# Optimization experiments

Measured on AMD Instinct MI355X. Metric: run time of the kernel, lower is better.

Reference implementation:

```python
import jax, jax.numpy as jnp
import numpy as np


def setup_inputs() -> dict:
    key = jax.random.key(0)
    kq, kk, kv, kb = jax.random.split(key, 4)
    B, H, S, D = 2, 12, 2048, 64
    q = jax.random.normal(kq, (B, H, S, D), dtype=jnp.float32)
    k = jax.random.normal(kk, (B, H, S, D), dtype=jnp.float32)
    v = jax.random.normal(kv, (B, H, S, D), dtype=jnp.float32)
    # sorted block ids -> contiguous blocks along the sequence
    block_ids = jnp.sort(jax.random.randint(kb, (B, S), 0, 4), axis=-1)
    return {"q": q, "k": k, "v": v, "block_ids": block_ids}


def _ghostmax(scores):
    # softmax over [scores, 0]: an extra ghost logit of value 0
    m = jnp.maximum(jnp.max(scores, axis=-1, keepdims=True), 0.0)
    e = jnp.exp(scores - m)
    denom = jnp.sum(e, axis=-1, keepdims=True) + jnp.exp(-m)
    return e / denom


def reference(q, k, v, block_ids):
    B, H, S, D = q.shape
    scaling = 1.0 / jnp.sqrt(jnp.asarray(D, dtype=q.dtype))
    # [B,H,S,S] scores
    scores = jnp.einsum('bhqd,bhkd->bhqk', q, k) * scaling
    # block-causal mask: attend only within same block AND to past positions
    same_block = block_ids[:, :, None] == block_ids[:, None, :]          # [B,S,S]
    causal = jnp.arange(S)[:, None] >= jnp.arange(S)[None, :]            # [S,S]
    mask = (same_block & causal)[:, None, :, :]                          # [B,1,S,S]
    scores = scores + (1.0 - mask.astype(scores.dtype)) * (-1e9)
    weights = _ghostmax(scores)
    # dropout p=0.0 (eval) -> identity
    return jnp.einsum('bhqk,bhkd->bhqd', weights, v)
```

## Files before the change

### kernel.cpp

```cpp
#include <hip/hip_runtime.h>


constexpr int Bc = 2, Hc = 12, Sc = 2048, Dc = 64;
constexpr int QT    = 16;
constexpr int LPR   = 4;
constexpr int DSUB  = 16;
constexpr int KTILE = 16;

__device__ __forceinline__ float bf_lo(unsigned u) {
    union { unsigned i; float f; } c; c.i = u << 16; return c.f;
}
__device__ __forceinline__ float bf_hi(unsigned u) {
    union { unsigned i; float f; } c; c.i = u & 0xffff0000u; return c.f;
}
__device__ __forceinline__ void expand_store(float* dst, float4 raw) {
    const unsigned* u = (const unsigned*)&raw;
    float4 a, b;
    a.x = bf_lo(u[0]); a.y = bf_hi(u[0]); a.z = bf_lo(u[1]); a.w = bf_hi(u[1]);
    b.x = bf_lo(u[2]); b.y = bf_hi(u[2]); b.z = bf_lo(u[3]); b.w = bf_hi(u[3]);
    ((float4*)dst)[0] = a;
    ((float4*)dst)[1] = b;
}

__global__ void sniff_dtype(const unsigned* __restrict__ q, int* __restrict__ flag) {
    __shared__ int acc;
    const int tid = threadIdx.x;
    if (tid == 0) acc = 0;
    __syncthreads();
    const unsigned word = q[tid];
    const int e = (word >> 7) & 0xff;
    const bool plausible = (e >= 0x70) && (e <= 0x90);
    const unsigned long long mask = __ballot(plausible);
    if ((tid & 63) == 0) atomicAdd(&acc, __popcll(mask));
    __syncthreads();
    if (tid == 0) *flag = (acc >= 128) ? 1 : 0;
}

template <bool BF16_IN>
__device__ __forceinline__ void attn_body(
    const void* __restrict__ qv, const void* __restrict__ kv_,
    const void* __restrict__ vv, const int* __restrict__ bidg,
    float* __restrict__ outg)
{
    __shared__ __align__(16) float ks[KTILE][Dc];
    __shared__ __align__(16) float vs[KTILE][Dc];
    __shared__ int kb[KTILE];

    const int bh    = blockIdx.x;
    const int qt    = blockIdx.y;
    const int b     = bh / Hc;
    const int tid   = threadIdx.x;
    const int q0    = qt * QT;
    const int r     = q0 + (tid >> 2);
    const int dbase = (tid & 3) * DSUB;

    const int* brow   = bidg + b * Sc;
    const int  my_bid = brow[r];
    const int  bid0   = brow[q0];

    int lo = 0, hi = q0;
    while (lo < hi) {
        int mid = (lo + hi) >> 1;
        if (brow[mid] < bid0) lo = mid + 1; else hi = mid;
    }
    const int kstart = lo & ~(KTILE - 1);
    const int ntiles = (q0 + QT - kstart) / KTILE;

    float qr[DSUB];
    if (BF16_IN) {
        const float4* qraw = (const float4*)((const unsigned short*)qv
                              + ((size_t)bh * Sc + r) * Dc + dbase);
        #pragma unroll
        for (int i = 0; i < 2; ++i) {
            float4 rw = qraw[i];
            const unsigned* u = (const unsigned*)&rw;
            #pragma unroll
            for (int j = 0; j < 4; ++j) {
                qr[i * 8 + 2 * j + 0] = bf_lo(u[j]) * 0.125f;
                qr[i * 8 + 2 * j + 1] = bf_hi(u[j]) * 0.125f;
            }
        }
    } else {
        const float4* qraw = (const float4*)((const float*)qv
                              + ((size_t)bh * Sc + r) * Dc + dbase);
        #pragma unroll
        for (int i = 0; i < 4; ++i) {
            float4 t = qraw[i];
            qr[4*i+0] = t.x * 0.125f; qr[4*i+1] = t.y * 0.125f;
            qr[4*i+2] = t.z * 0.125f; qr[4*i+3] = t.w * 0.125f;
        }
    }

    float o[DSUB];
    #pragma unroll
    for (int d = 0; d < DSUB; ++d) o[d] = 0.f;
    float m = -1e30f;
    float l = 0.f;

    const float4* kbase = BF16_IN
        ? (const float4*)((const unsigned short*)kv_ + (size_t)bh * Sc * Dc)
        : (const float4*)((const float*)kv_ + (size_t)bh * Sc * Dc);
    const float4* vbase = BF16_IN
        ? (const float4*)((const unsigned short*)vv + (size_t)bh * Sc * Dc)
        : (const float4*)((const float*)vv + (size_t)bh * Sc * Dc);

    for (int t = 0; t < ntiles; ++t) {
        const int kt = kstart + t * KTILE;

        __syncthreads();
        if (BF16_IN) {
            #pragma unroll
            for (int i = 0; i < 2; ++i) {
                expand_store(&ks[0][0] + 8 * (tid + i * 64), kbase[kt * 8 + tid + i * 64]);
                expand_store(&vs[0][0] + 8 * (tid + i * 64), vbase[kt * 8 + tid + i * 64]);
            }
        } else {
            float4* kd = (float4*)&ks[0][0];
            float4* vd = (float4*)&vs[0][0];
            #pragma unroll
            for (int i = 0; i < 4; ++i) {
                kd[tid + i * 64] = kbase[kt * 16 + tid + i * 64];
                vd[tid + i * 64] = vbase[kt * 16 + tid + i * 64];
            }
        }
        if (tid < KTILE) kb[tid] = brow[kt + tid];
        __syncthreads();

        for (int kk = 0; kk < KTILE; ++kk) {
            const float4* krow4 = (const float4*)(&ks[kk][dbase]);
            float s0 = 0.f, s1 = 0.f, s2 = 0.f, s3 = 0.f;
            #pragma unroll
            for (int i = 0; i < DSUB / 4; ++i) {
                float4 kv4 = krow4[i];
                s0 = fmaf(qr[4*i+0], kv4.x, s0);
                s1 = fmaf(qr[4*i+1], kv4.y, s1);
                s2 = fmaf(qr[4*i+2], kv4.z, s2);
                s3 = fmaf(qr[4*i+3], kv4.w, s3);
            }
            float s = (s0 + s1) + (s2 + s3);
            s += __shfl_xor(s, 1);
            s += __shfl_xor(s, 2);

            const int  kgi   = kt + kk;
            const bool valid = (kgi <= r) && (kb[kk] == my_bid);
            if (valid) {
                if (s > m) {
                    const float c = __expf(m - s);
                    l *= c;
                    #pragma unroll
                    for (int d = 0; d < DSUB; ++d) o[d] *= c;
                    m = s;
                }
                const float e = __expf(s - m);
                l += e;
                const float4* vrow = (const float4*)(&vs[kk][dbase]);
                #pragma unroll
                for (int i = 0; i < DSUB / 4; ++i) {
                    float4 vv4 = vrow[i];
                    o[4*i+0] = fmaf(e, vv4.x, o[4*i+0]);
                    o[4*i+1] = fmaf(e, vv4.y, o[4*i+1]);
                    o[4*i+2] = fmaf(e, vv4.z, o[4*i+2]);
                    o[4*i+3] = fmaf(e, vv4.w, o[4*i+3]);
                }
            }
        }
    }

    const float Mg    = fmaxf(m, 0.f);
    const float c     = __expf(m - Mg);
    const float denom = l * c + __expf(-Mg);
    const float scale = c / denom;

    float4* orow = (float4*)(outg + ((size_t)bh * Sc + r) * Dc + dbase);
    #pragma unroll
    for (int i = 0; i < 4; ++i) {
        float4 t;
        t.x = o[4*i+0] * scale; t.y = o[4*i+1] * scale;
        t.z = o[4*i+2] * scale; t.w = o[4*i+3] * scale;
        orow[i] = t;
    }
}

__global__ __launch_bounds__(64) void block_causal_attn(
    const void* __restrict__ qv, const void* __restrict__ kv_,
    const void* __restrict__ vv, const int* __restrict__ bidg,
    float* __restrict__ outg, const int* __restrict__ flag)
{
    if (*flag)
        attn_body<true >(qv, kv_, vv, bidg, outg);
    else
        attn_body<false>(qv, kv_, vv, bidg, outg);
}

extern "C" void kernel_launch(void* const* d_in, const int* in_sizes, int n_in,
                              void* d_out, int out_size, void* d_ws, size_t ws_size,
                              hipStream_t stream) {
    const void* q    = d_in[0];
    const void* k    = d_in[1];
    const void* v    = d_in[2];
    const int*  bids = (const int*)d_in[3];
    float*      out  = (float*)d_out;
    int*        flag = (int*)d_ws;

    sniff_dtype<<<1, 256, 0, stream>>>((const unsigned*)q, flag);
    dim3 grid(Bc * Hc, Sc / QT);
    block_causal_attn<<<grid, dim3(64), 0, stream>>>(q, k, v, bids, out, flag);
}
```

Baseline: 292.5 us.

## Prefetch next K/V tile into registers and batch per-tile online softmax

Loads the next K/V tile into registers while the current tile is computed, so global load latency overlaps with compute. The per-key branchy online softmax becomes a per-tile step: all 16 scores are computed, one max and one rescale are applied per tile, and then branch-free exp and PV accumulation follow. Query tiles are also launched in reverse order so the longest causal tiles start first. In exchange, register pressure goes up, and masked keys now cost a full PV FMA instead of being skipped.

New measurement: 267.3 us. -8.6%, faster.

```diff
diff --git a/kernel.cpp b/kernel.cpp
--- a/kernel.cpp
+++ b/kernel.cpp
@@ -3,7 +3,6 @@
 
 constexpr int Bc = 2, Hc = 12, Sc = 2048, Dc = 64;
 constexpr int QT    = 16;
-constexpr int LPR   = 4;
 constexpr int DSUB  = 16;
 constexpr int KTILE = 16;
 
@@ -47,7 +46,7 @@
     __shared__ int kb[KTILE];
 
     const int bh    = blockIdx.x;
-    const int qt    = blockIdx.y;
+    const int qt    = (gridDim.y - 1) - blockIdx.y;
     const int b     = bh / Hc;
     const int tid   = threadIdx.x;
     const int q0    = qt * QT;
@@ -103,6 +102,15 @@
     const float4* vbase = BF16_IN
         ? (const float4*)((const unsigned short*)vv + (size_t)bh * Sc * Dc)
         : (const float4*)((const float*)vv + (size_t)bh * Sc * Dc);
+    constexpr int NR    = BF16_IN ? 2 : 4;
+    constexpr int ROWF4 = BF16_IN ? 8 : 16;
+
+    float4 kreg[NR], vreg[NR];
+    #pragma unroll
+    for (int j = 0; j < NR; ++j) {
+        kreg[j] = kbase[kstart * ROWF4 + tid + j * 64];
+        vreg[j] = vbase[kstart * ROWF4 + tid + j * 64];
+    }
 
     for (int t = 0; t < ntiles; ++t) {
         const int kt = kstart + t * KTILE;
@@ -110,22 +118,34 @@
         __syncthreads();
         if (BF16_IN) {
             #pragma unroll
-            for (int i = 0; i < 2; ++i) {
-                expand_store(&ks[0][0] + 8 * (tid + i * 64), kbase[kt * 8 + tid + i * 64]);
-                expand_store(&vs[0][0] + 8 * (tid + i * 64), vbase[kt * 8 + tid + i * 64]);
+            for (int j = 0; j < NR; ++j) {
+                expand_store(&ks[0][0] + 8 * (tid + j * 64), kreg[j]);
+                expand_store(&vs[0][0] + 8 * (tid + j * 64), vreg[j]);
             }
         } else {
             float4* kd = (float4*)&ks[0][0];
             float4* vd = (float4*)&vs[0][0];
             #pragma unroll
-            for (int i = 0; i < 4; ++i) {
-                kd[tid + i * 64] = kbase[kt * 16 + tid + i * 64];
-                vd[tid + i * 64] = vbase[kt * 16 + tid + i * 64];
+            for (int j = 0; j < NR; ++j) {
+                kd[tid + j * 64] = kreg[j];
+                vd[tid + j * 64] = vreg[j];
             }
         }
         if (tid < KTILE) kb[tid] = brow[kt + tid];
         __syncthreads();
 
+        if (t + 1 < ntiles) {
+            const int ktn = kt + KTILE;
+            #pragma unroll
+            for (int j = 0; j < NR; ++j) {
+                kreg[j] = kbase[ktn * ROWF4 + tid + j * 64];
+                vreg[j] = vbase[ktn * ROWF4 + tid + j * 64];
+            }
+        }
+
+        float s[KTILE];
+        unsigned vmask = 0;
+        #pragma unroll
         for (int kk = 0; kk < KTILE; ++kk) {
             const float4* krow4 = (const float4*)(&ks[kk][dbase]);
             float s0 = 0.f, s1 = 0.f, s2 = 0.f, s3 = 0.f;
@@ -137,39 +157,52 @@
                 s2 = fmaf(qr[4*i+2], kv4.z, s2);
                 s3 = fmaf(qr[4*i+3], kv4.w, s3);
             }
-            float s = (s0 + s1) + (s2 + s3);
-            s += __shfl_xor(s, 1);
-            s += __shfl_xor(s, 2);
+            float sv = (s0 + s1) + (s2 + s3);
+            sv += __shfl_xor(sv, 1);
+            sv += __shfl_xor(sv, 2);
 
             const int  kgi   = kt + kk;
             const bool valid = (kgi <= r) && (kb[kk] == my_bid);
-            if (valid) {
-                if (s > m) {
-                    const float c = __expf(m - s);
-                    l *= c;
-                    #pragma unroll
-                    for (int d = 0; d < DSUB; ++d) o[d] *= c;
-                    m = s;
-                }
-                const float e = __expf(s - m);
-                l += e;
-                const float4* vrow = (const float4*)(&vs[kk][dbase]);
-                #pragma unroll
-                for (int i = 0; i < DSUB / 4; ++i) {
-                    float4 vv4 = vrow[i];
-                    o[4*i+0] = fmaf(e, vv4.x, o[4*i+0]);
-                    o[4*i+1] = fmaf(e, vv4.y, o[4*i+1]);
-                    o[4*i+2] = fmaf(e, vv4.z, o[4*i+2]);
-                    o[4*i+3] = fmaf(e, vv4.w, o[4*i+3]);
-                }
+            vmask |= (valid ? 1u : 0u) << kk;
+            s[kk] = valid ? sv : -1e30f;
+        }
+
+        float pmax = s[0];
+        #pragma unroll
+        for (int kk = 1; kk < KTILE; ++kk) pmax = fmaxf(pmax, s[kk]);
+        const float M = fmaxf(m, pmax);
+        const float c = __expf(m - M);
+        l *= c;
+        #pragma unroll
+        for (int d = 0; d < DSUB; ++d) o[d] *= c;
+        m = M;
+
+        #pragma unroll
+        for (int kk = 0; kk < KTILE; ++kk) {
+            const float e = ((vmask >> kk) & 1u) ? __expf(s[kk] - m) : 0.f;
+            l += e;
+            s[kk] = e;
+        }
+
+        #pragma unroll
+        for (int kk = 0; kk < KTILE; ++kk) {
+            const float e = s[kk];
+            const float4* vrow = (const float4*)(&vs[kk][dbase]);
+            #pragma unroll
+            for (int i = 0; i < DSUB / 4; ++i) {
+                float4 vv4 = vrow[i];
+                o[4*i+0] = fmaf(e, vv4.x, o[4*i+0]);
+                o[4*i+1] = fmaf(e, vv4.y, o[4*i+1]);
+                o[4*i+2] = fmaf(e, vv4.z, o[4*i+2]);
+                o[4*i+3] = fmaf(e, vv4.w, o[4*i+3]);
             }
         }
     }
 
     const float Mg    = fmaxf(m, 0.f);
-    const float c     = __expf(m - Mg);
-    const float denom = l * c + __expf(-Mg);
-    const float scale = c / denom;
+    const float cg    = __expf(m - Mg);
+    const float denom = l * cg + __expf(-Mg);
+    const float scale = cg / denom;
 
     float4* orow = (float4*)(outg + ((size_t)bh * Sc + r) * Dc + dbase);
     #pragma unroll
```
